# Kernel optimization log

Hardware: AMD Instinct MI355X
Metric: run time of the kernel (lower is better)

## Reference

```python
import jax, jax.numpy as jnp
import numpy as np

NH = 4; HD = 128; C = 512; GRID = 14; L = GRID * GRID  # 196 tokens

def _rel_index():
    ch = np.arange(GRID)
    coords = np.stack(np.meshgrid(ch, ch, indexing='ij')).reshape(2, -1)  # [2, L_grid]
    rel = (coords[:, :, None] - coords[:, None, :]).transpose(1, 2, 0).copy()  # [L,L,2]
    rel[:, :, 0] += GRID - 1
    rel[:, :, 1] += GRID - 1
    rel[:, :, 0] *= 2 * GRID - 1
    return rel.sum(-1)  # [L,L] in [0, (2*GRID-1)^2)

REL_IDX = jnp.asarray(_rel_index())

def _pool7(x):
    # exact adaptive_avg_pool2d to (7,7): H,W are multiples of 7
    B, Cc, H, W = x.shape
    return x.reshape(B, Cc, 7, H // 7, 7, W // 7).mean(axis=(3, 5))

def _ln(x, g, b):
    m = x.mean(-1, keepdims=True)
    v = ((x - m) ** 2).mean(-1, keepdims=True)
    return (x - m) / jnp.sqrt(v + 1e-5) * g + b

def _attn(x, qkv_w, qkv_b, bt, pw, pb):
    B, Lx, Cx = x.shape
    qkv = (x @ qkv_w + qkv_b).reshape(B, Lx, 3, NH, HD).transpose(2, 0, 3, 1, 4)
    q, k, v = qkv[0] * (HD ** -0.5), qkv[1], qkv[2]  # [B,NH,L,HD]
    attn = jnp.einsum('bhld,bhmd->bhlm', q, k)
    bias = bt[REL_IDX]  # gather: [L,L,NH]
    attn = jax.nn.softmax(attn + bias.transpose(2, 0, 1)[None], axis=-1)
    o = jnp.einsum('bhlm,bhmd->bhld', attn, v).transpose(0, 2, 1, 3).reshape(B, Lx, Cx)
    return o @ pw + pb

def _layer(x, ln1_g, ln1_b, qkv_w, qkv_b, bt, pw, pb, ln2_g, ln2_b, w1, b1, w2, b2):
    x = x + _attn(_ln(x, ln1_g, ln1_b), qkv_w, qkv_b, bt, pw, pb)
    h = _ln(x, ln2_g, ln2_b)
    return x + jax.nn.relu(h @ w1 + b1) @ w2 + b2


def setup_inputs() -> dict:
    key = jax.random.key(0)
    ks = iter(jax.random.split(key, 40))
    chans = [96, 192, 384, 768]
    sizes = [56, 28, 14, 7]
    B = 64
    d = {}
    for i, (c, s) in enumerate(zip(chans, sizes)):
        d[f'feat{i}'] = jax.random.normal(next(ks), (B, c, s, s), jnp.float32)
    for i, c in enumerate(chans):
        d[f'proj_w{i}'] = jax.random.normal(next(ks), (C, c), jnp.float32) * 0.02
        d[f'proj_b{i}'] = jnp.zeros((C,), jnp.float32)
    NL = 2
    d['ln1_g'] = jnp.ones((NL, C)); d['ln1_b'] = jnp.zeros((NL, C))
    d['qkv_w'] = jax.random.normal(next(ks), (NL, C, 3 * C), jnp.float32) * 0.02
    d['qkv_b'] = jnp.zeros((NL, 3 * C))
    d['bias_table'] = jax.random.normal(next(ks), (NL, (2 * GRID - 1) ** 2, NH), jnp.float32) * 0.02
    d['attn_pw'] = jax.random.normal(next(ks), (NL, C, C), jnp.float32) * 0.02
    d['attn_pb'] = jnp.zeros((NL, C))
    d['ln2_g'] = jnp.ones((NL, C)); d['ln2_b'] = jnp.zeros((NL, C))
    d['mlp_w1'] = jax.random.normal(next(ks), (NL, C, 4 * C), jnp.float32) * 0.02
    d['mlp_b1'] = jnp.zeros((NL, 4 * C))
    d['mlp_w2'] = jax.random.normal(next(ks), (NL, 4 * C, C), jnp.float32) * 0.02
    d['mlp_b2'] = jnp.zeros((NL, C))
    return d


def reference(feat0, feat1, feat2, feat3,
              proj_w0, proj_b0, proj_w1, proj_b1, proj_w2, proj_b2, proj_w3, proj_b3,
              ln1_g, ln1_b, qkv_w, qkv_b, bias_table, attn_pw, attn_pb,
              ln2_g, ln2_b, mlp_w1, mlp_b1, mlp_w2, mlp_b2):
    feats = [feat0, feat1, feat2, feat3]
    pws = [proj_w0, proj_w1, proj_w2, proj_w3]
    pbs = [proj_b0, proj_b1, proj_b2, proj_b3]
    tokens = []
    for f, w, b in zip(feats, pws, pbs):
        p = _pool7(f)  # [B,Cin,7,7]
        t = jnp.einsum('bchw,oc->bhwo', p, w) + b  # 1x1 conv -> channels-last
        tokens.append(t.reshape(t.shape[0], 49, C))
    x = jnp.concatenate(tokens, axis=1)  # [B,196,512]
    for l in range(ln1_g.shape[0]):
        x = _layer(x, ln1_g[l], ln1_b[l], qkv_w[l], qkv_b[l], bias_table[l],
                   attn_pw[l], attn_pb[l], ln2_g[l], ln2_b[l],
                   mlp_w1[l], mlp_b1[l], mlp_w2[l], mlp_b2[l])
    return x.mean(axis=1)  # [B,512]
```

## Files before the change

### kernel.cpp

```cpp
#include <hip/hip_runtime.h>
#include <hip/hip_bf16.h>

typedef __attribute__((ext_vector_type(8))) short short8;
typedef __attribute__((ext_vector_type(4))) float f32x4;

__device__ __forceinline__ unsigned short f2bf(float x) {
    unsigned int u = __builtin_bit_cast(unsigned int, x);
    unsigned int r = (u + 0x7FFFu + ((u >> 16) & 1u)) >> 16;
    return (unsigned short)r;
}

__device__ __forceinline__ void gload_lds16(const unsigned short* g, unsigned short* l) {
    __builtin_amdgcn_global_load_lds(
        (const __attribute__((address_space(1))) unsigned int*)g,
        (__attribute__((address_space(3))) unsigned int*)l, 16, 0, 0);
}

__global__ __launch_bounds__(256, 1) void gemm_wide(
    const unsigned short* __restrict__ A, int lda,
    const unsigned short* __restrict__ B, int ldb,
    const float* __restrict__ bias,
    int K,
    unsigned short* q_out, unsigned short* k_out, unsigned short* v_out,
    float qscale)
{
    int bx = blockIdx.x, by = blockIdx.y;
    {
        const int gx = gridDim.x;
        const int total = gx * gridDim.y;
        const int orig = by * gx + bx;
        const int q = total >> 3, r = total & 7;
        const int xcd = orig & 7, idx = orig >> 3;
        const int nf = (xcd < r ? xcd * (q + 1) : r * (q + 1) + (xcd - r) * q) + idx;
        bx = nf % gx;
        by = nf / gx;
    }
    const int bm = by * 128;
    const int bn = bx * 256;

    __shared__ unsigned short As[3][128][32];
    __shared__ unsigned short Bs[3][256][32];

    const int tid  = threadIdx.x;
    const int lane = tid & 63;
    const int wid  = tid >> 6;
    const int slot = lane >> 4;
    const int lcol = lane & 15;

    const int srow = tid >> 2;
    const int sgrn = tid & 3;
    const int scol_dst = sgrn * 8;
    const int scol_src = (sgrn ^ ((srow >> 1) & 3)) * 8;
    const int rslot = (slot ^ ((lcol >> 1) & 3)) * 8;

    const unsigned short* pa0 = A + (long long)(bm + srow) * lda + scol_src;
    const unsigned short* pa1 = A + (long long)(bm + 64 + srow) * lda + scol_src;
    const unsigned short* pb0 = B + (long long)(bn + srow) * ldb + scol_src;
    const unsigned short* pb1 = B + (long long)(bn + 64 + srow) * ldb + scol_src;
    const unsigned short* pb2 = B + (long long)(bn + 128 + srow) * ldb + scol_src;
    const unsigned short* pb3 = B + (long long)(bn + 192 + srow) * ldb + scol_src;

    f32x4 acc[8][4];
    #pragma unroll
    for (int i = 0; i < 8; ++i)
        #pragma unroll
        for (int j = 0; j < 4; ++j)
            acc[i][j] = (f32x4){0.f, 0.f, 0.f, 0.f};

    const int nt = K >> 5;

    gload_lds16(pa0, &As[0][srow][scol_dst]);
    gload_lds16(pa1, &As[0][64 + srow][scol_dst]);
    gload_lds16(pb0, &Bs[0][srow][scol_dst]);
    gload_lds16(pb1, &Bs[0][64 + srow][scol_dst]);
    gload_lds16(pb2, &Bs[0][128 + srow][scol_dst]);
    gload_lds16(pb3, &Bs[0][192 + srow][scol_dst]);
    gload_lds16(pa0 + 32, &As[1][srow][scol_dst]);
    gload_lds16(pa1 + 32, &As[1][64 + srow][scol_dst]);
    gload_lds16(pb0 + 32, &Bs[1][srow][scol_dst]);
    gload_lds16(pb1 + 32, &Bs[1][64 + srow][scol_dst]);
    gload_lds16(pb2 + 32, &Bs[1][128 + srow][scol_dst]);
    gload_lds16(pb3 + 32, &Bs[1][192 + srow][scol_dst]);

    int cur = 0;
    for (int t = 0; t < nt; ++t) {
        const int nxt2 = t + 2;
        if (nxt2 < nt) {
            const int nb = nxt2 % 3;
            const long long koff = (long long)nxt2 << 5;
            gload_lds16(pa0 + koff, &As[nb][srow][scol_dst]);
            gload_lds16(pa1 + koff, &As[nb][64 + srow][scol_dst]);
            gload_lds16(pb0 + koff, &Bs[nb][srow][scol_dst]);
            gload_lds16(pb1 + koff, &Bs[nb][64 + srow][scol_dst]);
            gload_lds16(pb2 + koff, &Bs[nb][128 + srow][scol_dst]);
            gload_lds16(pb3 + koff, &Bs[nb][192 + srow][scol_dst]);
        }
        if (nxt2 < nt)          asm volatile("s_waitcnt vmcnt(12)" ::: "memory");
        else if (t + 1 < nt)    asm volatile("s_waitcnt vmcnt(6)" ::: "memory");
        else                    asm volatile("s_waitcnt vmcnt(0)" ::: "memory");
        __builtin_amdgcn_s_barrier();
        __builtin_amdgcn_sched_barrier(0);

        short8 afr[8], bfr[4];
        #pragma unroll
        for (int mi = 0; mi < 8; ++mi)
            afr[mi] = *(const short8*)&As[cur][mi * 16 + lcol][rslot];
        #pragma unroll
        for (int ni = 0; ni < 4; ++ni)
            bfr[ni] = *(const short8*)&Bs[cur][wid * 64 + ni * 16 + lcol][rslot];
        #pragma unroll
        for (int mi = 0; mi < 8; ++mi)
            #pragma unroll
            for (int ni = 0; ni < 4; ++ni)
                acc[mi][ni] = __builtin_amdgcn_mfma_f32_16x16x32_bf16(
                    afr[mi], bfr[ni], acc[mi][ni], 0, 0, 0);

        __builtin_amdgcn_s_barrier();
        cur = (cur == 2) ? 0 : cur + 1;
    }

    #pragma unroll
    for (int mi = 0; mi < 8; ++mi) {
        int rbase = bm + mi * 16 + slot * 4;
        #pragma unroll
        for (int ni = 0; ni < 4; ++ni) {
            int gc = bn + wid * 64 + ni * 16 + lcol;
            float bv = bias[gc];
            f32x4 a = acc[mi][ni];
            int which = gc >> 9;
            int hh = (gc >> 7) & 3;
            int d  = gc & 127;
            #pragma unroll
            for (int rr = 0; rr < 4; ++rr) {
                int gr = rbase + rr;
                float v = a[rr] + bv;
                int b_ = gr / 196, l_ = gr % 196;
                int zz = b_ * 4 + hh;
                if (which == 0)
                    q_out[((long long)zz * 196 + l_) * 128 + d] = f2bf(v * qscale);
                else if (which == 1)
                    k_out[((long long)zz * 196 + l_) * 128 + d] = f2bf(v);
                else
                    v_out[((long long)zz * 128 + d) * 224 + l_] = f2bf(v);
            }
        }
    }
}

__global__ __launch_bounds__(256) void gemm64(
    const unsigned short* __restrict__ A, int lda,
    const unsigned short* __restrict__ B, int ldb,
    void* __restrict__ Cv, int ldc,
    const float* __restrict__ bias,
    const float* __restrict__ res, int ldres,
    int K, int relu, int mode,
    unsigned short* q_out, unsigned short* k_out, unsigned short* v_out,
    float qscale)
{
    int bx = blockIdx.x, by = blockIdx.y;
    {
        const int gx = gridDim.x;
        const int total = gx * gridDim.y;
        if ((total & 7) == 0) {
            const int orig = by * gx + bx;
            const int per = total >> 3;
            const int nf = (orig & 7) * per + (orig >> 3);
            bx = nf % gx;
            by = nf / gx;
        }
    }
    const int bm = by * 128;
    const int bn = bx * 128;

    __shared__ unsigned short As[2][128][64];
    __shared__ unsigned short Bs[2][128][64];

    const int tid  = threadIdx.x;
    const int lane = tid & 63;
    const int wid  = tid >> 6;
    const int wm   = wid >> 1;
    const int wn   = wid & 1;
    const int slot = lane >> 4;
    const int lcol = lane & 15;

    const int trow = tid >> 3;
    const int tgrn = tid & 7;
    const int scol_dst = tgrn * 8;
    const int scol_src = (tgrn ^ (trow & 7)) * 8;

    const unsigned short* pa[4];
    const unsigned short* pb[4];
    #pragma unroll
    for (int p = 0; p < 4; ++p) {
        pa[p] = A + (long long)(bm + p * 32 + trow) * lda + scol_src;
        pb[p] = B + (long long)(bn + p * 32 + trow) * ldb + scol_src;
    }

    f32x4 acc[4][4];
    #pragma unroll
    for (int i = 0; i < 4; ++i)
        #pragma unroll
        for (int j = 0; j < 4; ++j)
            acc[i][j] = (f32x4){0.f, 0.f, 0.f, 0.f};

    const int nt = K >> 6;

    #pragma unroll
    for (int p = 0; p < 4; ++p) {
        gload_lds16(pa[p], &As[0][p * 32 + trow][scol_dst]);
        gload_lds16(pb[p], &Bs[0][p * 32 + trow][scol_dst]);
    }
    __syncthreads();

    for (int t = 0; t < nt; ++t) {
        const int cur = t & 1;
        if (t + 1 < nt) {
            const int nb = (t + 1) & 1;
            const long long koff = (long long)(t + 1) << 6;
            #pragma unroll
            for (int p = 0; p < 4; ++p) {
                gload_lds16(pa[p] + koff, &As[nb][p * 32 + trow][scol_dst]);
                gload_lds16(pb[p] + koff, &Bs[nb][p * 32 + trow][scol_dst]);
            }
        }

        short8 afr[4][2], bfr[4][2];
        #pragma unroll
        for (int mi = 0; mi < 4; ++mi) {
            const int row = wm * 64 + mi * 16 + lcol;
            #pragma unroll
            for (int ks = 0; ks < 2; ++ks) {
                const int g = ((ks * 4 + slot) ^ (lcol & 7)) * 8;
                afr[mi][ks] = *(const short8*)&As[cur][row][g];
            }
        }
        #pragma unroll
        for (int ni = 0; ni < 4; ++ni) {
            const int row = wn * 64 + ni * 16 + lcol;
            #pragma unroll
            for (int ks = 0; ks < 2; ++ks) {
                const int g = ((ks * 4 + slot) ^ (lcol & 7)) * 8;
                bfr[ni][ks] = *(const short8*)&Bs[cur][row][g];
            }
        }
        #pragma unroll
        for (int mi = 0; mi < 4; ++mi)
            #pragma unroll
            for (int ni = 0; ni < 4; ++ni)
                #pragma unroll
                for (int ks = 0; ks < 2; ++ks)
                    acc[mi][ni] = __builtin_amdgcn_mfma_f32_16x16x32_bf16(
                        afr[mi][ks], bfr[ni][ks], acc[mi][ni], 0, 0, 0);

        __syncthreads();
    }

    float* Cf = (float*)Cv;
    unsigned short* Cb = (unsigned short*)Cv;

    #pragma unroll
    for (int mi = 0; mi < 4; ++mi) {
        int rbase = bm + wm * 64 + mi * 16 + slot * 4;
        #pragma unroll
        for (int ni = 0; ni < 4; ++ni) {
            int gc = bn + wn * 64 + ni * 16 + lcol;
            float bv = bias ? bias[gc] : 0.f;
            f32x4 a = acc[mi][ni];
            #pragma unroll
            for (int rr = 0; rr < 4; ++rr) {
                int gr = rbase + rr;
                float v = a[rr] + bv;
                if (mode == 0) {
                    if (res) v += res[(long long)gr * ldres + gc];
                    if (relu) v = fmaxf(v, 0.f);
                    Cf[(long long)gr * ldc + gc] = v;
                } else {
                    if (relu) v = fmaxf(v, 0.f);
                    Cb[(long long)gr * ldc + gc] = f2bf(v);
                }
            }
        }
    }
}

__global__ __launch_bounds__(256) void gemm_bf16(
    const unsigned short* __restrict__ A, long long sA, int lda,
    const unsigned short* __restrict__ B, long long sB, int ldb,
    void* __restrict__ Cv, long long sC, int ldc,
    const float* __restrict__ bias,
    const float* __restrict__ res, int ldres,
    int M, int N, int K,
    int relu, int mode, int rowoff,
    unsigned short* q_out, unsigned short* k_out, unsigned short* v_out,
    float qscale)
{
    const int z = blockIdx.z;
    A += (long long)z * sA;
    B += (long long)z * sB;

    const int bm = blockIdx.y * 128;
    const int bn = blockIdx.x * 128;

    __shared__ unsigned short As[3][128][32];
    __shared__ unsigned short Bs[3][128][32];

    const int tid  = threadIdx.x;
    const int lane = tid & 63;
    const int wid  = tid >> 6;
    const int wm   = wid >> 1;
    const int wn   = wid & 1;
    const int slot = lane >> 4;
    const int lcol = lane & 15;

    const int srow = tid >> 2;
    const int sgrn = tid & 3;
    const int scol_dst = sgrn * 8;
    const int scol_src = (sgrn ^ ((srow >> 1) & 3)) * 8;
    const int rslot = (slot ^ ((lcol >> 1) & 3)) * 8;

    int ga0 = bm + srow;       if (ga0 > M - 1) ga0 = M - 1;
    int ga1 = bm + 64 + srow;  if (ga1 > M - 1) ga1 = M - 1;
    int gb0 = bn + srow;       if (gb0 > N - 1) gb0 = N - 1;
    int gb1 = bn + 64 + srow;  if (gb1 > N - 1) gb1 = N - 1;
    const unsigned short* pa0 = A + (long long)ga0 * lda + scol_src;
    const unsigned short* pa1 = A + (long long)ga1 * lda + scol_src;
    const unsigned short* pb0 = B + (long long)gb0 * ldb + scol_src;
    const unsigned short* pb1 = B + (long long)gb1 * ldb + scol_src;

    f32x4 acc[4][4];
    #pragma unroll
    for (int i = 0; i < 4; ++i)
        #pragma unroll
        for (int j = 0; j < 4; ++j)
            acc[i][j] = (f32x4){0.f, 0.f, 0.f, 0.f};

    const int nt = K >> 5;

    gload_lds16(pa0, &As[0][srow][scol_dst]);
    gload_lds16(pa1, &As[0][64 + srow][scol_dst]);
    gload_lds16(pb0, &Bs[0][srow][scol_dst]);
    gload_lds16(pb1, &Bs[0][64 + srow][scol_dst]);
    if (nt > 1) {
        gload_lds16(pa0 + 32, &As[1][srow][scol_dst]);
        gload_lds16(pa1 + 32, &As[1][64 + srow][scol_dst]);
        gload_lds16(pb0 + 32, &Bs[1][srow][scol_dst]);
        gload_lds16(pb1 + 32, &Bs[1][64 + srow][scol_dst]);
    }

    int cur = 0;
    for (int t = 0; t < nt; ++t) {
        const int nxt2 = t + 2;
        if (nxt2 < nt) {
            const int nb = nxt2 % 3;
            const long long koff = (long long)nxt2 << 5;
            gload_lds16(pa0 + koff, &As[nb][srow][scol_dst]);
            gload_lds16(pa1 + koff, &As[nb][64 + srow][scol_dst]);
            gload_lds16(pb0 + koff, &Bs[nb][srow][scol_dst]);
            gload_lds16(pb1 + koff, &Bs[nb][64 + srow][scol_dst]);
        }
        if (nxt2 < nt)          asm volatile("s_waitcnt vmcnt(8)" ::: "memory");
        else if (t + 1 < nt)    asm volatile("s_waitcnt vmcnt(4)" ::: "memory");
        else                    asm volatile("s_waitcnt vmcnt(0)" ::: "memory");
        __builtin_amdgcn_s_barrier();
        __builtin_amdgcn_sched_barrier(0);

        short8 afr[4], bfr[4];
        #pragma unroll
        for (int mi = 0; mi < 4; ++mi)
            afr[mi] = *(const short8*)&As[cur][wm * 64 + mi * 16 + lcol][rslot];
        #pragma unroll
        for (int ni = 0; ni < 4; ++ni)
            bfr[ni] = *(const short8*)&Bs[cur][wn * 64 + ni * 16 + lcol][rslot];
        #pragma unroll
        for (int mi = 0; mi < 4; ++mi)
            #pragma unroll
            for (int ni = 0; ni < 4; ++ni)
                acc[mi][ni] = __builtin_amdgcn_mfma_f32_16x16x32_bf16(
                    afr[mi], bfr[ni], acc[mi][ni], 0, 0, 0);

        __builtin_amdgcn_s_barrier();
        cur = (cur == 2) ? 0 : cur + 1;
    }

    float* Cf = (float*)Cv + (mode == 0 ? (long long)z * sC : 0);

    #pragma unroll
    for (int mi = 0; mi < 4; ++mi) {
        int rbase = bm + wm * 64 + mi * 16 + slot * 4;
        #pragma unroll
        for (int ni = 0; ni < 4; ++ni) {
            int gc = bn + wn * 64 + ni * 16 + lcol;
            if (gc >= N) continue;
            float bv = bias ? bias[gc] : 0.f;
            f32x4 a = acc[mi][ni];
            #pragma unroll
            for (int rr = 0; rr < 4; ++rr) {
                int gr = rbase + rr;
                if (gr >= M) continue;
                float v = a[rr] + bv;
                if (mode == 0) {
                    if (res) v += res[(long long)gr * ldres + gc];
                    if (relu) v = fmaxf(v, 0.f);
                    Cf[(long long)gr * ldc + gc] = v;
                } else {
                    int orow = (gr / 49) * 196 + rowoff + (gr % 49);
                    Cf[(long long)orow * ldc + gc] = v;
                }
            }
        }
    }
}

__global__ __launch_bounds__(256) void flash_k(
    const unsigned short* __restrict__ q_bf,
    const unsigned short* __restrict__ k_bf,
    const unsigned short* __restrict__ v_t,
    unsigned short* __restrict__ O,
    const float* __restrict__ bt)
{
    const int z = blockIdx.x;
    const int h = z & 3, bb = z >> 2;
    const int tid = threadIdx.x;
    const int w = tid >> 6;
    const int lane = tid & 63;
    const int slot = lane >> 4;
    const int lcol = lane & 15;

    __shared__ unsigned short Ps[4][16][68];

    const unsigned short* Qz = q_bf + (long long)z * 196 * 128;
    const unsigned short* Kz = k_bf + (long long)z * 196 * 128;
    const unsigned short* Vz = v_t  + (long long)z * 128 * 224;

    short8 qf[4][4];
    #pragma unroll
    for (int i = 0; i < 4; ++i) {
        const int row = (w + 4 * i) * 16 + lcol;
        #pragma unroll
        for (int ks = 0; ks < 4; ++ks)
            qf[i][ks] = *(const short8*)(Qz + (long long)row * 128 + ks * 32 + slot * 8);
    }

    f32x4 o[4][8];
    #pragma unroll
    for (int i = 0; i < 4; ++i)
        #pragma unroll
        for (int nd = 0; nd < 8; ++nd)
            o[i][nd] = (f32x4){0.f, 0.f, 0.f, 0.f};

    float m_r[4][4], l_r[4][4];
    #pragma unroll
    for (int i = 0; i < 4; ++i)
        #pragma unroll
        for (int r = 0; r < 4; ++r) { m_r[i][r] = -3e38f; l_r[i][r] = 0.f; }

    int qi1[4][4], qj1[4][4];
    #pragma unroll
    for (int i = 0; i < 4; ++i)
        #pragma unroll
        for (int r = 0; r < 4; ++r) {
            int q = (w + 4 * i) * 16 + slot * 4 + r;
            int qq = q < 195 ? q : 195;
            qi1[i][r] = qq / 14;
            qj1[i][r] = qq % 14;
        }

    #pragma unroll
    for (int kt = 0; kt < 4; ++kt) {
        const int nkj  = (kt == 3) ? 2 : 4;
        const int nksl = (kt == 3) ? 1 : 2;

        short8 kf[4][4];
        #pragma unroll
        for (int kj = 0; kj < 4; ++kj) {
            if (kj >= nkj) continue;
            const int krow = kt * 64 + kj * 16 + lcol;
            #pragma unroll
            for (int ks = 0; ks < 4; ++ks)
                kf[kj][ks] = *(const short8*)(Kz + (long long)krow * 128 + ks * 32 + slot * 8);
        }

        f32x4 s[4][4];
        __builtin_amdgcn_s_setprio(1);
        #pragma unroll
        for (int i = 0; i < 4; ++i)
            #pragma unroll
            for (int kj = 0; kj < 4; ++kj) {
                if (kj >= nkj) continue;
                f32x4 a = (f32x4){0.f, 0.f, 0.f, 0.f};
                #pragma unroll
                for (int ks = 0; ks < 4; ++ks)
                    a = __builtin_amdgcn_mfma_f32_16x16x32_bf16(qf[i][ks], kf[kj][ks], a, 0, 0, 0);
                s[i][kj] = a;
            }
        __builtin_amdgcn_s_setprio(0);

        short8 vf[8][2];
        #pragma unroll
        for (int nd = 0; nd < 8; ++nd)
            #pragma unroll
            for (int ksl = 0; ksl < 2; ++ksl) {
                if (ksl >= nksl) continue;
                vf[nd][ksl] = *(const short8*)(Vz + (long long)(nd * 16 + lcol) * 224
                                               + kt * 64 + ksl * 32 + slot * 8);
            }

        #pragma unroll
        for (int i = 0; i < 4; ++i) {
            #pragma unroll
            for (int kj = 0; kj < 4; ++kj) {
                if (kj >= nkj) continue;
                const int key = kt * 64 + kj * 16 + lcol;
                const int kk = key < 195 ? key : 195;
                const int i2 = kk / 14, j2 = kk % 14;
                #pragma unroll
                for (int r = 0; r < 4; ++r) {
                    const int idx = (qi1[i][r] - i2 + 13) * 27 + (qj1[i][r] - j2 + 13);
                    float sv = s[i][kj][r] + bt[idx * 4 + h];
                    if (key >= 196) sv = -3e38f;
                    s[i][kj][r] = sv;
                }
            }
            f32x4 pm = s[i][0];
            #pragma unroll
            for (int kj = 1; kj < 4; ++kj) {
                if (kj >= nkj) continue;
                #pragma unroll
                for (int r = 0; r < 4; ++r) pm[r] = fmaxf(pm[r], s[i][kj][r]);
            }
            #pragma unroll
            for (int r = 0; r < 4; ++r) {
                #pragma unroll
                for (int off = 1; off < 16; off <<= 1)
                    pm[r] = fmaxf(pm[r], __shfl_xor(pm[r], off));
            }
            float sf[4];
            #pragma unroll
            for (int r = 0; r < 4; ++r) {
                float mn = fmaxf(m_r[i][r], pm[r]);
                sf[r] = __expf(m_r[i][r] - mn);
                m_r[i][r] = mn;
            }
            f32x4 ladd = (f32x4){0.f, 0.f, 0.f, 0.f};
            #pragma unroll
            for (int kj = 0; kj < 4; ++kj) {
                if (kj >= nkj) continue;
                #pragma unroll
                for (int r = 0; r < 4; ++r) {
                    float p = __expf(s[i][kj][r] - m_r[i][r]);
                    s[i][kj][r] = p;
                    ladd[r] += p;
                }
            }
            #pragma unroll
            for (int r = 0; r < 4; ++r) {
                #pragma unroll
                for (int off = 1; off < 16; off <<= 1)
                    ladd[r] += __shfl_xor(ladd[r], off);
                l_r[i][r] = l_r[i][r] * sf[r] + ladd[r];
            }
            #pragma unroll
            for (int nd = 0; nd < 8; ++nd)
                #pragma unroll
                for (int r = 0; r < 4; ++r) o[i][nd][r] *= sf[r];
            #pragma unroll
            for (int kj = 0; kj < 4; ++kj) {
                if (kj >= nkj) continue;
                #pragma unroll
                for (int r = 0; r < 4; ++r)
                    Ps[w][slot * 4 + r][kj * 16 + lcol] = f2bf(s[i][kj][r]);
            }
            __builtin_amdgcn_s_setprio(1);
            #pragma unroll
            for (int ksl = 0; ksl < 2; ++ksl) {
                if (ksl >= nksl) continue;
                short8 pa = *(const short8*)&Ps[w][lcol][ksl * 32 + slot * 8];
                #pragma unroll
                for (int nd = 0; nd < 8; ++nd)
                    o[i][nd] = __builtin_amdgcn_mfma_f32_16x16x32_bf16(pa, vf[nd][ksl], o[i][nd], 0, 0, 0);
            }
            __builtin_amdgcn_s_setprio(0);
        }
    }

    #pragma unroll
    for (int i = 0; i < 4; ++i) {
        #pragma unroll
        for (int r = 0; r < 4; ++r) {
            const int q = (w + 4 * i) * 16 + slot * 4 + r;
            if (q >= 196) continue;
            const float rn = 1.f / l_r[i][r];
            unsigned short* op = O + ((long long)(bb * 196 + q)) * 512 + h * 128 + lcol;
            #pragma unroll
            for (int nd = 0; nd < 8; ++nd)
                op[nd * 16] = f2bf(o[i][nd][r] * rn);
        }
    }
}

__global__ __launch_bounds__(256) void wconv_t(const float* __restrict__ W,
                                               unsigned short* __restrict__ Wt,
                                               int K, int N)
{
    W  += (long long)blockIdx.z * K * N;
    Wt += (long long)blockIdx.z * K * N;
    __shared__ float t[32][33];
    int tx = threadIdx.x & 31, ty = threadIdx.x >> 5;
    int n0 = blockIdx.x * 32, k0 = blockIdx.y * 32;
    #pragma unroll
    for (int j = 0; j < 4; ++j)
        t[ty + j * 8][tx] = W[(long long)(k0 + ty + j * 8) * N + n0 + tx];
    __syncthreads();
    #pragma unroll
    for (int j = 0; j < 4; ++j)
        Wt[(long long)(n0 + ty + j * 8) * K + k0 + tx] = f2bf(t[tx][ty + j * 8]);
}

__global__ __launch_bounds__(256) void wcv_k(const float* __restrict__ in,
                                             unsigned short* __restrict__ out, int n)
{
    int i = blockIdx.x * 256 + threadIdx.x;
    if (i < n) out[i] = f2bf(in[i]);
}

template<int F>
__global__ __launch_bounds__(256) void pool_k(const float* __restrict__ feat,
                                              unsigned short* __restrict__ P, int ch)
{
    const int S = 7 * F;
    int wv = blockIdx.x * 4 + (threadIdx.x >> 6);
    int lane = threadIdx.x & 63;
    int b = wv / ch, c = wv % ch;
    if (lane >= 49) return;
    int oh = lane / 7, ow = lane % 7;
    const float* src = feat + ((long long)b * ch + c) * (S * S) + (oh * F) * S + ow * F;
    float acc = 0.f;
    #pragma unroll
    for (int hh = 0; hh < F; ++hh) {
        const float* row = src + hh * S;
        if constexpr (F == 8) {
            float4 a = *(const float4*)row;
            float4 d = *(const float4*)(row + 4);
            acc += a.x + a.y + a.z + a.w + d.x + d.y + d.z + d.w;
        } else if constexpr (F == 4) {
            float4 a = *(const float4*)row;
            acc += a.x + a.y + a.z + a.w;
        } else if constexpr (F == 2) {
            float2 a = *(const float2*)row;
            acc += a.x + a.y;
        } else {
            acc += row[0];
        }
    }
    P[((long long)(b * 49 + lane)) * ch + c] = f2bf(acc * (1.f / (F * F)));
}

__global__ __launch_bounds__(256) void ln_k(const float* __restrict__ x,
                                            unsigned short* __restrict__ y,
                                            const float* __restrict__ g,
                                            const float* __restrict__ b)
{
    long long row = blockIdx.x * 4 + (threadIdx.x >> 6);
    const float* xr = x + row * 512;
    unsigned short* yr = y + row * 512;
    int lane = threadIdx.x & 63;
    float v[8];
    float s = 0.f, ss = 0.f;
    #pragma unroll
    for (int p = 0; p < 8; ++p) {
        v[p] = xr[lane + p * 64];
        s += v[p]; ss += v[p] * v[p];
    }
    #pragma unroll
    for (int off = 32; off >= 1; off >>= 1) {
        s  += __shfl_xor(s, off);
        ss += __shfl_xor(ss, off);
    }
    float mean = s * (1.f / 512.f);
    float var  = ss * (1.f / 512.f) - mean * mean;
    float rstd = rsqrtf(var + 1e-5f);
    #pragma unroll
    for (int p = 0; p < 8; ++p) {
        int c = lane + p * 64;
        yr[c] = f2bf((v[p] - mean) * rstd * g[c] + b[c]);
    }
}

__global__ __launch_bounds__(512) void mean_k(const float* __restrict__ X,
                                              float* __restrict__ out)
{
    int b = blockIdx.x, c = threadIdx.x;
    const float* xp = X + (long long)b * 196 * 512 + c;
    float s = 0.f;
    for (int t = 0; t < 196; ++t) s += xp[t * 512];
    out[b * 512 + c] = s * (1.f / 196.f);
}

extern "C" void kernel_launch(void* const* d_in, const int* in_sizes, int n_in,
                              void* d_out, int out_size, void* d_ws, size_t ws_size,
                              hipStream_t stream)
{
    const float* feat[4]   = {(const float*)d_in[0], (const float*)d_in[1],
                              (const float*)d_in[2], (const float*)d_in[3]};
    const float* proj_w[4] = {(const float*)d_in[4], (const float*)d_in[6],
                              (const float*)d_in[8], (const float*)d_in[10]};
    const float* proj_b[4] = {(const float*)d_in[5], (const float*)d_in[7],
                              (const float*)d_in[9], (const float*)d_in[11]};
    const float* ln1_g = (const float*)d_in[12];
    const float* ln1_b = (const float*)d_in[13];
    const float* qkv_w = (const float*)d_in[14];
    const float* qkv_b = (const float*)d_in[15];
    const float* bias_table = (const float*)d_in[16];
    const float* attn_pw = (const float*)d_in[17];
    const float* attn_pb = (const float*)d_in[18];
    const float* ln2_g = (const float*)d_in[19];
    const float* ln2_b = (const float*)d_in[20];
    const float* mlp_w1 = (const float*)d_in[21];
    const float* mlp_b1 = (const float*)d_in[22];
    const float* mlp_w2 = (const float*)d_in[23];
    const float* mlp_b2 = (const float*)d_in[24];

    const long long NXT = 64LL * 196 * 512;

    float* X  = (float*)d_ws;
    float* S  = X + NXT;
    unsigned short* O_bf = (unsigned short*)S;

    unsigned short* ub    = (unsigned short*)(S + 256LL * 196 * 196);
    unsigned short* XN_bf = ub;
    unsigned short* q_bf  = XN_bf + NXT;
    unsigned short* k_bf  = q_bf + NXT;
    unsigned short* v_t   = k_bf + NXT;
    unsigned short* H     = q_bf;
    unsigned short* wts   = v_t + 256LL * 128 * 224 + 256LL * 196 * 224;

    unsigned short* qkvw_t = wts;
    unsigned short* pw_t   = qkvw_t + 2LL * 1536 * 512;
    unsigned short* w1_t   = pw_t   + 2LL * 512 * 512;
    unsigned short* w2_t   = w1_t   + 2LL * 2048 * 512;
    unsigned short* pjw    = w2_t   + 2LL * 512 * 2048;
    unsigned short* P_bf   = pjw + 512LL * (96 + 192 + 384 + 768);
    unsigned short* pjw_i[4];
    const int chans[4] = {96, 192, 384, 768};
    {
        unsigned short* p = pjw;
        for (int i = 0; i < 4; ++i) { pjw_i[i] = p; p += 512LL * chans[i]; }
    }

    wconv_t<<<dim3(1536/32, 512/32, 2), 256, 0, stream>>>(qkv_w, qkvw_t, 512, 1536);
    wconv_t<<<dim3(512/32, 512/32, 2), 256, 0, stream>>>(attn_pw, pw_t, 512, 512);
    wconv_t<<<dim3(2048/32, 512/32, 2), 256, 0, stream>>>(mlp_w1, w1_t, 512, 2048);
    wconv_t<<<dim3(512/32, 2048/32, 2), 256, 0, stream>>>(mlp_w2, w2_t, 2048, 512);
    for (int i = 0; i < 4; ++i) {
        int n = 512 * chans[i];
        wcv_k<<<(n + 255) / 256, 256, 0, stream>>>(proj_w[i], pjw_i[i], n);
    }

    pool_k<8><<<64 * 96  / 4, 256, 0, stream>>>(feat[0], P_bf, 96);
    gemm_bf16<<<dim3(4, 25, 1), 256, 0, stream>>>(
        P_bf, 0, 96, pjw_i[0], 0, 96, X, 0, 512, proj_b[0], nullptr, 0,
        3136, 512, 96, 0, 1, 0, nullptr, nullptr, nullptr, 0.f);
    pool_k<4><<<64 * 192 / 4, 256, 0, stream>>>(feat[1], P_bf, 192);
    gemm_bf16<<<dim3(4, 25, 1), 256, 0, stream>>>(
        P_bf, 0, 192, pjw_i[1], 0, 192, X, 0, 512, proj_b[1], nullptr, 0,
        3136, 512, 192, 0, 1, 49, nullptr, nullptr, nullptr, 0.f);
    pool_k<2><<<64 * 384 / 4, 256, 0, stream>>>(feat[2], P_bf, 384);
    gemm_bf16<<<dim3(4, 25, 1), 256, 0, stream>>>(
        P_bf, 0, 384, pjw_i[2], 0, 384, X, 0, 512, proj_b[2], nullptr, 0,
        3136, 512, 384, 0, 1, 98, nullptr, nullptr, nullptr, 0.f);
    pool_k<1><<<64 * 768 / 4, 256, 0, stream>>>(feat[3], P_bf, 768);
    gemm_bf16<<<dim3(4, 25, 1), 256, 0, stream>>>(
        P_bf, 0, 768, pjw_i[3], 0, 768, X, 0, 512, proj_b[3], nullptr, 0,
        3136, 512, 768, 0, 1, 147, nullptr, nullptr, nullptr, 0.f);

    for (int l = 0; l < 2; ++l) {
        ln_k<<<3136, 256, 0, stream>>>(X, XN_bf, ln1_g + l * 512, ln1_b + l * 512);

        gemm_wide<<<dim3(6, 98), 256, 0, stream>>>(
            XN_bf, 512,
            qkvw_t + (long long)l * 1536 * 512, 512,
            qkv_b + l * 1536,
            512,
            q_bf, k_bf, v_t, 0.08838834764831845f);

        flash_k<<<256, 256, 0, stream>>>(q_bf, k_bf, v_t, O_bf,
                                         bias_table + (long long)l * 729 * 4);

        gemm64<<<dim3(4, 98), 256, 0, stream>>>(
            O_bf, 512,
            pw_t + (long long)l * 512 * 512, 512,
            X, 512,
            attn_pb + l * 512, X, 512,
            512, 0, 0,
            nullptr, nullptr, nullptr, 0.f);

        ln_k<<<3136, 256, 0, stream>>>(X, XN_bf, ln2_g + l * 512, ln2_b + l * 512);

        gemm64<<<dim3(16, 98), 256, 0, stream>>>(
            XN_bf, 512,
            w1_t + (long long)l * 2048 * 512, 512,
            H, 2048,
            mlp_b1 + l * 2048, nullptr, 0,
            512, 1, 4,
            nullptr, nullptr, nullptr, 0.f);

        gemm64<<<dim3(4, 98), 256, 0, stream>>>(
            H, 2048,
            w2_t + (long long)l * 512 * 2048, 2048,
            X, 512,
            mlp_b2 + l * 512, X, 512,
            2048, 0, 0,
            nullptr, nullptr, nullptr, 0.f);
    }

    mean_k<<<64, 512, 0, stream>>>(X, (float*)d_out);
}
```

Before: 750.7 us.

## Batch four projection GEMMs into one launch and shrink QKV GEMM tiles

The four pooled-feature projection GEMMs, each previously run after its own pooling kernel on a shared buffer, now use separate pooled buffers. All pooling runs first, followed by one batched gemm_proj launch indexed by blockIdx.z, which removes serialization between pool and GEMM pairs. The wide 128x256 QKV GEMM is replaced by a 128x128 tile version with a 2x2 wave layout and twice as many blocks, trading per-block reuse for more parallelism and lower register pressure. The pooled buffers are placed inside the score scratch region at a fixed offset, which relies on that region being large enough.

```diff
diff --git a/kernel.cpp b/kernel.cpp
--- a/kernel.cpp
+++ b/kernel.cpp
@@ -16,11 +16,13 @@
         (__attribute__((address_space(3))) unsigned int*)l, 16, 0, 0);
 }
 
-__global__ __launch_bounds__(256, 1) void gemm_wide(
+__global__ __launch_bounds__(256) void gemm64(
     const unsigned short* __restrict__ A, int lda,
     const unsigned short* __restrict__ B, int ldb,
+    void* __restrict__ Cv, int ldc,
     const float* __restrict__ bias,
-    int K,
+    const float* __restrict__ res, int ldres,
+    int K, int relu, int mode,
     unsigned short* q_out, unsigned short* k_out, unsigned short* v_out,
     float qscale)
 {
@@ -28,22 +30,159 @@
     {
         const int gx = gridDim.x;
         const int total = gx * gridDim.y;
-        const int orig = by * gx + bx;
-        const int q = total >> 3, r = total & 7;
-        const int xcd = orig & 7, idx = orig >> 3;
-        const int nf = (xcd < r ? xcd * (q + 1) : r * (q + 1) + (xcd - r) * q) + idx;
-        bx = nf % gx;
-        by = nf / gx;
+        if ((total & 7) == 0) {
+            const int orig = by * gx + bx;
+            const int per = total >> 3;
+            const int nf = (orig & 7) * per + (orig >> 3);
+            bx = nf % gx;
+            by = nf / gx;
+        }
     }
     const int bm = by * 128;
-    const int bn = bx * 256;
-
-    __shared__ unsigned short As[3][128][32];
-    __shared__ unsigned short Bs[3][256][32];
+    const int bn = bx * 128;
+
+    __shared__ unsigned short As[2][128][64];
+    __shared__ unsigned short Bs[2][128][64];
 
     const int tid  = threadIdx.x;
     const int lane = tid & 63;
     const int wid  = tid >> 6;
+    const int wm   = wid >> 1;
+    const int wn   = wid & 1;
+    const int slot = lane >> 4;
+    const int lcol = lane & 15;
+
+    const int trow = tid >> 3;
+    const int tgrn = tid & 7;
+    const int scol_dst = tgrn * 8;
+    const int scol_src = (tgrn ^ (trow & 7)) * 8;
+
+    const unsigned short* pa[4];
+    const unsigned short* pb[4];
+    #pragma unroll
+    for (int p = 0; p < 4; ++p) {
+        pa[p] = A + (long long)(bm + p * 32 + trow) * lda + scol_src;
+        pb[p] = B + (long long)(bn + p * 32 + trow) * ldb + scol_src;
+    }
+
+    f32x4 acc[4][4];
+    #pragma unroll
+    for (int i = 0; i < 4; ++i)
+        #pragma unroll
+        for (int j = 0; j < 4; ++j)
+            acc[i][j] = (f32x4){0.f, 0.f, 0.f, 0.f};
+
+    const int nt = K >> 6;
+
+    #pragma unroll
+    for (int p = 0; p < 4; ++p) {
+        gload_lds16(pa[p], &As[0][p * 32 + trow][scol_dst]);
+        gload_lds16(pb[p], &Bs[0][p * 32 + trow][scol_dst]);
+    }
+    __syncthreads();
+
+    for (int t = 0; t < nt; ++t) {
+        const int cur = t & 1;
+        if (t + 1 < nt) {
+            const int nb = (t + 1) & 1;
+            const long long koff = (long long)(t + 1) << 6;
+            #pragma unroll
+            for (int p = 0; p < 4; ++p) {
+                gload_lds16(pa[p] + koff, &As[nb][p * 32 + trow][scol_dst]);
+                gload_lds16(pb[p] + koff, &Bs[nb][p * 32 + trow][scol_dst]);
+            }
+        }
+
+        short8 afr[4][2], bfr[4][2];
+        #pragma unroll
+        for (int mi = 0; mi < 4; ++mi) {
+            const int row = wm * 64 + mi * 16 + lcol;
+            #pragma unroll
+            for (int ks = 0; ks < 2; ++ks) {
+                const int g = ((ks * 4 + slot) ^ (lcol & 7)) * 8;
+                afr[mi][ks] = *(const short8*)&As[cur][row][g];
+            }
+        }
+        #pragma unroll
+        for (int ni = 0; ni < 4; ++ni) {
+            const int row = wn * 64 + ni * 16 + lcol;
+            #pragma unroll
+            for (int ks = 0; ks < 2; ++ks) {
+                const int g = ((ks * 4 + slot) ^ (lcol & 7)) * 8;
+                bfr[ni][ks] = *(const short8*)&Bs[cur][row][g];
+            }
+        }
+        #pragma unroll
+        for (int mi = 0; mi < 4; ++mi)
+            #pragma unroll
+            for (int ni = 0; ni < 4; ++ni)
+                #pragma unroll
+                for (int ks = 0; ks < 2; ++ks)
+                    acc[mi][ni] = __builtin_amdgcn_mfma_f32_16x16x32_bf16(
+                        afr[mi][ks], bfr[ni][ks], acc[mi][ni], 0, 0, 0);
+
+        __syncthreads();
+    }
+
+    float* Cf = (float*)Cv;
+    unsigned short* Cb = (unsigned short*)Cv;
+
+    #pragma unroll
+    for (int mi = 0; mi < 4; ++mi) {
+        int rbase = bm + wm * 64 + mi * 16 + slot * 4;
+        #pragma unroll
+        for (int ni = 0; ni < 4; ++ni) {
+            int gc = bn + wn * 64 + ni * 16 + lcol;
+            float bv = bias ? bias[gc] : 0.f;
+            f32x4 a = acc[mi][ni];
+            #pragma unroll
+            for (int rr = 0; rr < 4; ++rr) {
+                int gr = rbase + rr;
+                float v = a[rr] + bv;
+                if (mode == 0) {
+                    if (res) v += res[(long long)gr * ldres + gc];
+                    if (relu) v = fmaxf(v, 0.f);
+                    Cf[(long long)gr * ldc + gc] = v;
+                } else {
+                    if (relu) v = fmaxf(v, 0.f);
+                    Cb[(long long)gr * ldc + gc] = f2bf(v);
+                }
+            }
+        }
+    }
+}
+
+__global__ __launch_bounds__(256) void gemm_bf16(
+    const unsigned short* __restrict__ A, int lda,
+    const unsigned short* __restrict__ B, int ldb,
+    const float* __restrict__ bias,
+    int M, int N, int K,
+    unsigned short* q_out, unsigned short* k_out, unsigned short* v_out,
+    float qscale)
+{
+    int bx = blockIdx.x, by = blockIdx.y;
+    {
+        const int gx = gridDim.x;
+        const int total = gx * gridDim.y;
+        if ((total & 7) == 0) {
+            const int orig = by * gx + bx;
+            const int per = total >> 3;
+            const int nf = (orig & 7) * per + (orig >> 3);
+            bx = nf % gx;
+            by = nf / gx;
+        }
+    }
+    const int bm = by * 128;
+    const int bn = bx * 128;
+
+    __shared__ unsigned short As[3][128][32];
+    __shared__ unsigned short Bs[3][128][32];
+
+    const int tid  = threadIdx.x;
+    const int lane = tid & 63;
+    const int wid  = tid >> 6;
+    const int wm   = wid >> 1;
+    const int wn   = wid & 1;
     const int slot = lane >> 4;
     const int lcol = lane & 15;
 
@@ -57,12 +196,10 @@
     const unsigned short* pa1 = A + (long long)(bm + 64 + srow) * lda + scol_src;
     const unsigned short* pb0 = B + (long long)(bn + srow) * ldb + scol_src;
     const unsigned short* pb1 = B + (long long)(bn + 64 + srow) * ldb + scol_src;
-    const unsigned short* pb2 = B + (long long)(bn + 128 + srow) * ldb + scol_src;
-    const unsigned short* pb3 = B + (long long)(bn + 192 + srow) * ldb + scol_src;
-
-    f32x4 acc[8][4];
-    #pragma unroll
-    for (int i = 0; i < 8; ++i)
+
+    f32x4 acc[4][4];
+    #pragma unroll
+    for (int i = 0; i < 4; ++i)
         #pragma unroll
         for (int j = 0; j < 4; ++j)
             acc[i][j] = (f32x4){0.f, 0.f, 0.f, 0.f};
@@ -73,14 +210,12 @@
     gload_lds16(pa1, &As[0][64 + srow][scol_dst]);
     gload_lds16(pb0, &Bs[0][srow][scol_dst]);
     gload_lds16(pb1, &Bs[0][64 + srow][scol_dst]);
-    gload_lds16(pb2, &Bs[0][128 + srow][scol_dst]);
-    gload_lds16(pb3, &Bs[0][192 + srow][scol_dst]);
-    gload_lds16(pa0 + 32, &As[1][srow][scol_dst]);
-    gload_lds16(pa1 + 32, &As[1][64 + srow][scol_dst]);
-    gload_lds16(pb0 + 32, &Bs[1][srow][scol_dst]);
-    gload_lds16(pb1 + 32, &Bs[1][64 + srow][scol_dst]);
-    gload_lds16(pb2 + 32, &Bs[1][128 + srow][scol_dst]);
-    gload_lds16(pb3 + 32, &Bs[1][192 + srow][scol_dst]);
+    if (nt > 1) {
+        gload_lds16(pa0 + 32, &As[1][srow][scol_dst]);
+        gload_lds16(pa1 + 32, &As[1][64 + srow][scol_dst]);
+        gload_lds16(pb0 + 32, &Bs[1][srow][scol_dst]);
+        gload_lds16(pb1 + 32, &Bs[1][64 + srow][scol_dst]);
+    }
 
     int cur = 0;
     for (int t = 0; t < nt; ++t) {
@@ -92,24 +227,22 @@
             gload_lds16(pa1 + koff, &As[nb][64 + srow][scol_dst]);
             gload_lds16(pb0 + koff, &Bs[nb][srow][scol_dst]);
             gload_lds16(pb1 + koff, &Bs[nb][64 + srow][scol_dst]);
-            gload_lds16(pb2 + koff, &Bs[nb][128 + srow][scol_dst]);
-            gload_lds16(pb3 + koff, &Bs[nb][192 + srow][scol_dst]);
-        }
-        if (nxt2 < nt)          asm volatile("s_waitcnt vmcnt(12)" ::: "memory");
-        else if (t + 1 < nt)    asm volatile("s_waitcnt vmcnt(6)" ::: "memory");
+        }
+        if (nxt2 < nt)          asm volatile("s_waitcnt vmcnt(8)" ::: "memory");
+        else if (t + 1 < nt)    asm volatile("s_waitcnt vmcnt(4)" ::: "memory");
         else                    asm volatile("s_waitcnt vmcnt(0)" ::: "memory");
         __builtin_amdgcn_s_barrier();
         __builtin_amdgcn_sched_barrier(0);
 
-        short8 afr[8], bfr[4];
-        #pragma unroll
-        for (int mi = 0; mi < 8; ++mi)
-            afr[mi] = *(const short8*)&As[cur][mi * 16 + lcol][rslot];
+        short8 afr[4], bfr[4];
+        #pragma unroll
+        for (int mi = 0; mi < 4; ++mi)
+            afr[mi] = *(const short8*)&As[cur][wm * 64 + mi * 16 + lcol][rslot];
         #pragma unroll
         for (int ni = 0; ni < 4; ++ni)
-            bfr[ni] = *(const short8*)&Bs[cur][wid * 64 + ni * 16 + lcol][rslot];
-        #pragma unroll
-        for (int mi = 0; mi < 8; ++mi)
+            bfr[ni] = *(const short8*)&Bs[cur][wn * 64 + ni * 16 + lcol][rslot];
+        #pragma unroll
+        for (int mi = 0; mi < 4; ++mi)
             #pragma unroll
             for (int ni = 0; ni < 4; ++ni)
                 acc[mi][ni] = __builtin_amdgcn_mfma_f32_16x16x32_bf16(
@@ -120,11 +253,11 @@
     }
 
     #pragma unroll
-    for (int mi = 0; mi < 8; ++mi) {
-        int rbase = bm + mi * 16 + slot * 4;
+    for (int mi = 0; mi < 4; ++mi) {
+        int rbase = bm + wm * 64 + mi * 16 + slot * 4;
         #pragma unroll
         for (int ni = 0; ni < 4; ++ni) {
-            int gc = bn + wid * 64 + ni * 16 + lcol;
+            int gc = bn + wn * 64 + ni * 16 + lcol;
             float bv = bias[gc];
             f32x4 a = acc[mi][ni];
             int which = gc >> 9;
@@ -147,33 +280,32 @@
     }
 }
 
-__global__ __launch_bounds__(256) void gemm64(
-    const unsigned short* __restrict__ A, int lda,
-    const unsigned short* __restrict__ B, int ldb,
-    void* __restrict__ Cv, int ldc,
-    const float* __restrict__ bias,
-    const float* __restrict__ res, int ldres,
-    int K, int relu, int mode,
-    unsigned short* q_out, unsigned short* k_out, unsigned short* v_out,
-    float qscale)
-{
-    int bx = blockIdx.x, by = blockIdx.y;
-    {
-        const int gx = gridDim.x;
-        const int total = gx * gridDim.y;
-        if ((total & 7) == 0) {
-            const int orig = by * gx + bx;
-            const int per = total >> 3;
-            const int nf = (orig & 7) * per + (orig >> 3);
-            bx = nf % gx;
-            by = nf / gx;
-        }
-    }
-    const int bm = by * 128;
-    const int bn = bx * 128;
-
-    __shared__ unsigned short As[2][128][64];
-    __shared__ unsigned short Bs[2][128][64];
+struct ProjArgs {
+    const unsigned short* P0; const unsigned short* P1;
+    const unsigned short* P2; const unsigned short* P3;
+    const unsigned short* W0; const unsigned short* W1;
+    const unsigned short* W2; const unsigned short* W3;
+    const float* b0; const float* b1; const float* b2; const float* b3;
+};
+
+__global__ __launch_bounds__(256) void gemm_proj(ProjArgs args, float* __restrict__ C)
+{
+    const int zi = blockIdx.z;
+    const unsigned short* A; const unsigned short* B; const float* bias;
+    int K;
+    if (zi == 0)      { A = args.P0; B = args.W0; bias = args.b0; K = 96;  }
+    else if (zi == 1) { A = args.P1; B = args.W1; bias = args.b1; K = 192; }
+    else if (zi == 2) { A = args.P2; B = args.W2; bias = args.b2; K = 384; }
+    else              { A = args.P3; B = args.W3; bias = args.b3; K = 768; }
+    const int rowoff = 49 * zi;
+    const int M = 3136, N = 512;
+    const int lda = K, ldb = K;
+
+    const int bm = blockIdx.y * 128;
+    const int bn = blockIdx.x * 128;
+
+    __shared__ unsigned short As[3][128][32];
+    __shared__ unsigned short Bs[3][128][32];
 
     const int tid  = threadIdx.x;
     const int lane = tid & 63;
@@ -183,135 +315,6 @@
     const int slot = lane >> 4;
     const int lcol = lane & 15;
 
-    const int trow = tid >> 3;
-    const int tgrn = tid & 7;
-    const int scol_dst = tgrn * 8;
-    const int scol_src = (tgrn ^ (trow & 7)) * 8;
-
-    const unsigned short* pa[4];
-    const unsigned short* pb[4];
-    #pragma unroll
-    for (int p = 0; p < 4; ++p) {
-        pa[p] = A + (long long)(bm + p * 32 + trow) * lda + scol_src;
-        pb[p] = B + (long long)(bn + p * 32 + trow) * ldb + scol_src;
-    }
-
-    f32x4 acc[4][4];
-    #pragma unroll
-    for (int i = 0; i < 4; ++i)
-        #pragma unroll
-        for (int j = 0; j < 4; ++j)
-            acc[i][j] = (f32x4){0.f, 0.f, 0.f, 0.f};
-
-    const int nt = K >> 6;
-
-    #pragma unroll
-    for (int p = 0; p < 4; ++p) {
-        gload_lds16(pa[p], &As[0][p * 32 + trow][scol_dst]);
-        gload_lds16(pb[p], &Bs[0][p * 32 + trow][scol_dst]);
-    }
-    __syncthreads();
-
-    for (int t = 0; t < nt; ++t) {
-        const int cur = t & 1;
-        if (t + 1 < nt) {
-            const int nb = (t + 1) & 1;
-            const long long koff = (long long)(t + 1) << 6;
-            #pragma unroll
-            for (int p = 0; p < 4; ++p) {
-                gload_lds16(pa[p] + koff, &As[nb][p * 32 + trow][scol_dst]);
-                gload_lds16(pb[p] + koff, &Bs[nb][p * 32 + trow][scol_dst]);
-            }
-        }
-
-        short8 afr[4][2], bfr[4][2];
-        #pragma unroll
-        for (int mi = 0; mi < 4; ++mi) {
-            const int row = wm * 64 + mi * 16 + lcol;
-            #pragma unroll
-            for (int ks = 0; ks < 2; ++ks) {
-                const int g = ((ks * 4 + slot) ^ (lcol & 7)) * 8;
-                afr[mi][ks] = *(const short8*)&As[cur][row][g];
-            }
-        }
-        #pragma unroll
-        for (int ni = 0; ni < 4; ++ni) {
-            const int row = wn * 64 + ni * 16 + lcol;
-            #pragma unroll
-            for (int ks = 0; ks < 2; ++ks) {
-                const int g = ((ks * 4 + slot) ^ (lcol & 7)) * 8;
-                bfr[ni][ks] = *(const short8*)&Bs[cur][row][g];
-            }
-        }
-        #pragma unroll
-        for (int mi = 0; mi < 4; ++mi)
-            #pragma unroll
-            for (int ni = 0; ni < 4; ++ni)
-                #pragma unroll
-                for (int ks = 0; ks < 2; ++ks)
-                    acc[mi][ni] = __builtin_amdgcn_mfma_f32_16x16x32_bf16(
-                        afr[mi][ks], bfr[ni][ks], acc[mi][ni], 0, 0, 0);
-
-        __syncthreads();
-    }
-
-    float* Cf = (float*)Cv;
-    unsigned short* Cb = (unsigned short*)Cv;
-
-    #pragma unroll
-    for (int mi = 0; mi < 4; ++mi) {
-        int rbase = bm + wm * 64 + mi * 16 + slot * 4;
-        #pragma unroll
-        for (int ni = 0; ni < 4; ++ni) {
-            int gc = bn + wn * 64 + ni * 16 + lcol;
-            float bv = bias ? bias[gc] : 0.f;
-            f32x4 a = acc[mi][ni];
-            #pragma unroll
-            for (int rr = 0; rr < 4; ++rr) {
-                int gr = rbase + rr;
-                float v = a[rr] + bv;
-                if (mode == 0) {
-                    if (res) v += res[(long long)gr * ldres + gc];
-                    if (relu) v = fmaxf(v, 0.f);
-                    Cf[(long long)gr * ldc + gc] = v;
-                } else {
-                    if (relu) v = fmaxf(v, 0.f);
-                    Cb[(long long)gr * ldc + gc] = f2bf(v);
-                }
-            }
-        }
-    }
-}
-
-__global__ __launch_bounds__(256) void gemm_bf16(
-    const unsigned short* __restrict__ A, long long sA, int lda,
-    const unsigned short* __restrict__ B, long long sB, int ldb,
-    void* __restrict__ Cv, long long sC, int ldc,
-    const float* __restrict__ bias,
-    const float* __restrict__ res, int ldres,
-    int M, int N, int K,
-    int relu, int mode, int rowoff,
-    unsigned short* q_out, unsigned short* k_out, unsigned short* v_out,
-    float qscale)
-{
-    const int z = blockIdx.z;
-    A += (long long)z * sA;
-    B += (long long)z * sB;
-
-    const int bm = blockIdx.y * 128;
-    const int bn = blockIdx.x * 128;
-
-    __shared__ unsigned short As[3][128][32];
-    __shared__ unsigned short Bs[3][128][32];
-
-    const int tid  = threadIdx.x;
-    const int lane = tid & 63;
-    const int wid  = tid >> 6;
-    const int wm   = wid >> 1;
-    const int wn   = wid & 1;
-    const int slot = lane >> 4;
-    const int lcol = lane & 15;
-
     const int srow = tid >> 2;
     const int sgrn = tid & 3;
     const int scol_dst = sgrn * 8;
@@ -320,12 +323,10 @@
 
     int ga0 = bm + srow;       if (ga0 > M - 1) ga0 = M - 1;
     int ga1 = bm + 64 + srow;  if (ga1 > M - 1) ga1 = M - 1;
-    int gb0 = bn + srow;       if (gb0 > N - 1) gb0 = N - 1;
-    int gb1 = bn + 64 + srow;  if (gb1 > N - 1) gb1 = N - 1;
     const unsigned short* pa0 = A + (long long)ga0 * lda + scol_src;
     const unsigned short* pa1 = A + (long long)ga1 * lda + scol_src;
-    const unsigned short* pb0 = B + (long long)gb0 * ldb + scol_src;
-    const unsigned short* pb1 = B + (long long)gb1 * ldb + scol_src;
+    const unsigned short* pb0 = B + (long long)(bn + srow) * ldb + scol_src;
+    const unsigned short* pb1 = B + (long long)(bn + 64 + srow) * ldb + scol_src;
 
     f32x4 acc[4][4];
     #pragma unroll
@@ -340,12 +341,10 @@
     gload_lds16(pa1, &As[0][64 + srow][scol_dst]);
     gload_lds16(pb0, &Bs[0][srow][scol_dst]);
     gload_lds16(pb1, &Bs[0][64 + srow][scol_dst]);
-    if (nt > 1) {
-        gload_lds16(pa0 + 32, &As[1][srow][scol_dst]);
-        gload_lds16(pa1 + 32, &As[1][64 + srow][scol_dst]);
-        gload_lds16(pb0 + 32, &Bs[1][srow][scol_dst]);
-        gload_lds16(pb1 + 32, &Bs[1][64 + srow][scol_dst]);
-    }
+    gload_lds16(pa0 + 32, &As[1][srow][scol_dst]);
+    gload_lds16(pa1 + 32, &As[1][64 + srow][scol_dst]);
+    gload_lds16(pb0 + 32, &Bs[1][srow][scol_dst]);
+    gload_lds16(pb1 + 32, &Bs[1][64 + srow][scol_dst]);
 
     int cur = 0;
     for (int t = 0; t < nt; ++t) {
@@ -382,30 +381,21 @@
         cur = (cur == 2) ? 0 : cur + 1;
     }
 
-    float* Cf = (float*)Cv + (mode == 0 ? (long long)z * sC : 0);
-
     #pragma unroll
     for (int mi = 0; mi < 4; ++mi) {
         int rbase = bm + wm * 64 + mi * 16 + slot * 4;
         #pragma unroll
         for (int ni = 0; ni < 4; ++ni) {
             int gc = bn + wn * 64 + ni * 16 + lcol;
-            if (gc >= N) continue;
-            float bv = bias ? bias[gc] : 0.f;
+            float bv = bias[gc];
             f32x4 a = acc[mi][ni];
             #pragma unroll
             for (int rr = 0; rr < 4; ++rr) {
                 int gr = rbase + rr;
                 if (gr >= M) continue;
                 float v = a[rr] + bv;
-                if (mode == 0) {
-                    if (res) v += res[(long long)gr * ldres + gc];
-                    if (relu) v = fmaxf(v, 0.f);
-                    Cf[(long long)gr * ldc + gc] = v;
-                } else {
-                    int orow = (gr / 49) * 196 + rowoff + (gr % 49);
-                    Cf[(long long)orow * ldc + gc] = v;
-                }
+                int orow = (gr / 49) * 196 + rowoff + (gr % 49);
+                C[(long long)orow * 512 + gc] = v;
             }
         }
     }
@@ -726,6 +716,14 @@
     float* S  = X + NXT;
     unsigned short* O_bf = (unsigned short*)S;
 
+    unsigned short* Sreg = (unsigned short*)S;
+    unsigned short* Pb[4];
+    {
+        unsigned short* p = Sreg + 7000000LL;
+        const int chs[4] = {96, 192, 384, 768};
+        for (int i = 0; i < 4; ++i) { Pb[i] = p; p += 3136LL * chs[i]; }
+    }
+
     unsigned short* ub    = (unsigned short*)(S + 256LL * 196 * 196);
     unsigned short* XN_bf = ub;
     unsigned short* q_bf  = XN_bf + NXT;
@@ -739,7 +737,6 @@
     unsigned short* w1_t   = pw_t   + 2LL * 512 * 512;
     unsigned short* w2_t   = w1_t   + 2LL * 2048 * 512;
     unsigned short* pjw    = w2_t   + 2LL * 512 * 2048;
-    unsigned short* P_bf   = pjw + 512LL * (96 + 192 + 384 + 768);
     unsigned short* pjw_i[4];
     const int chans[4] = {96, 192, 384, 768};
     {
@@ -756,31 +753,26 @@
         wcv_k<<<(n + 255) / 256, 256, 0, stream>>>(proj_w[i], pjw_i[i], n);
     }
 
-    pool_k<8><<<64 * 96  / 4, 256, 0, stream>>>(feat[0], P_bf, 96);
-    gemm_bf16<<<dim3(4, 25, 1), 256, 0, stream>>>(
-        P_bf, 0, 96, pjw_i[0], 0, 96, X, 0, 512, proj_b[0], nullptr, 0,
-        3136, 512, 96, 0, 1, 0, nullptr, nullptr, nullptr, 0.f);
-    pool_k<4><<<64 * 192 / 4, 256, 0, stream>>>(feat[1], P_bf, 192);
-    gemm_bf16<<<dim3(4, 25, 1), 256, 0, stream>>>(
-        P_bf, 0, 192, pjw_i[1], 0, 192, X, 0, 512, proj_b[1], nullptr, 0,
-        3136, 512, 192, 0, 1, 49, nullptr, nullptr, nullptr, 0.f);
-    pool_k<2><<<64 * 384 / 4, 256, 0, stream>>>(feat[2], P_bf, 384);
-    gemm_bf16<<<dim3(4, 25, 1), 256, 0, stream>>>(
-        P_bf, 0, 384, pjw_i[2], 0, 384, X, 0, 512, proj_b[2], nullptr, 0,
-        3136, 512, 384, 0, 1, 98, nullptr, nullptr, nullptr, 0.f);
-    pool_k<1><<<64 * 768 / 4, 256, 0, stream>>>(feat[3], P_bf, 768);
-    gemm_bf16<<<dim3(4, 25, 1), 256, 0, stream>>>(
-        P_bf, 0, 768, pjw_i[3], 0, 768, X, 0, 512, proj_b[3], nullptr, 0,
-        3136, 512, 768, 0, 1, 147, nullptr, nullptr, nullptr, 0.f);
+    pool_k<8><<<64 * 96  / 4, 256, 0, stream>>>(feat[0], Pb[0], 96);
+    pool_k<4><<<64 * 192 / 4, 256, 0, stream>>>(feat[1], Pb[1], 192);
+    pool_k<2><<<64 * 384 / 4, 256, 0, stream>>>(feat[2], Pb[2], 384);
+    pool_k<1><<<64 * 768 / 4, 256, 0, stream>>>(feat[3], Pb[3], 768);
+    {
+        ProjArgs pa;
+        pa.P0 = Pb[0]; pa.P1 = Pb[1]; pa.P2 = Pb[2]; pa.P3 = Pb[3];
+        pa.W0 = pjw_i[0]; pa.W1 = pjw_i[1]; pa.W2 = pjw_i[2]; pa.W3 = pjw_i[3];
+        pa.b0 = proj_b[0]; pa.b1 = proj_b[1]; pa.b2 = proj_b[2]; pa.b3 = proj_b[3];
+        gemm_proj<<<dim3(4, 25, 4), 256, 0, stream>>>(pa, X);
+    }
 
     for (int l = 0; l < 2; ++l) {
         ln_k<<<3136, 256, 0, stream>>>(X, XN_bf, ln1_g + l * 512, ln1_b + l * 512);
 
-        gemm_wide<<<dim3(6, 98), 256, 0, stream>>>(
+        gemm_bf16<<<dim3(12, 98), 256, 0, stream>>>(
             XN_bf, 512,
             qkvw_t + (long long)l * 1536 * 512, 512,
             qkv_b + l * 1536,
-            512,
+            12544, 1536, 512,
             q_bf, k_bf, v_t, 0.08838834764831845f);
 
         flash_k<<<256, 256, 0, stream>>>(q_bf, k_bf, v_t, O_bf,
```

Result: faster. 640.9 us (-14.6%).
